# Kernel optimization log

Hardware: AMD Instinct MI355X
Metric: run time of the kernel (lower is better)

## Reference

```python
import jax, jax.numpy as jnp
import numpy as np

PI = 3.14159  # constant used in the torch module
N_QUBITS = 10
N_LAYERS = 4
B = 1024  # number of graphs


def _lin_init(k, fan_in, fan_out):
    k1, k2 = jax.random.split(k)
    s = 1.0 / np.sqrt(fan_in)
    W = jax.random.uniform(k1, (fan_in, fan_out), jnp.float32, -s, s)
    b = jax.random.uniform(k2, (fan_out,), jnp.float32, -s, s)
    return W, b


def setup_inputs():
    key = jax.random.key(0)
    ks = jax.random.split(key, 12)
    N, E, Fin, H, Emb = 32768, 131072, 128, 256, 128
    x = jax.random.normal(ks[0], (N, Fin), jnp.float32)
    edge_index = jax.random.randint(ks[1], (2, E), 0, N)
    batch = jnp.sort(jax.random.randint(ks[2], (N,), 0, B))
    edge_attr = jax.random.uniform(ks[3], (E, 4), dtype=jnp.float32)
    W1, b1 = _lin_init(ks[4], Fin, H)          # GCNConv 1
    W2, b2 = _lin_init(ks[5], H, Emb)          # GCNConv 2
    projW, projb = _lin_init(ks[6], Emb, N_QUBITS)
    vqc_weights = jax.random.uniform(ks[7], (N_LAYERS, N_QUBITS), jnp.float32, 0.0, 2 * np.pi)
    epW, epb = _lin_init(ks[8], 4, N_QUBITS - 1)
    cW1, cb1 = _lin_init(ks[9], Emb + N_QUBITS, 16)
    cW2, cb2 = _lin_init(ks[10], 16, 1)
    return dict(x=x, edge_index=edge_index, batch=batch, edge_attr=edge_attr,
                W1=W1, b1=b1, W2=W2, b2=b2, projW=projW, projb=projb,
                vqc_weights=vqc_weights, epW=epW, epb=epb,
                cW1=cW1, cb1=cb1, cW2=cW2, cb2=cb2)


def _gcn_conv(x, W, b, src, dst, n):
    # GCNConv with self-loops: sym-normalized aggregation of xW
    h = x @ W
    deg = jnp.zeros((n,), x.dtype).at[dst].add(1.0) + 1.0  # +1 self-loop
    dinv = jax.lax.rsqrt(deg)
    coef = (dinv[src] * dinv[dst])[:, None]
    agg = jnp.zeros_like(h).at[dst].add(h[src] * coef)
    return agg + h * (1.0 / deg)[:, None] + b


def _segment_mean(v, seg, n):
    tot = jnp.zeros((n, v.shape[1]), v.dtype).at[seg].add(v)
    cnt = jnp.zeros((n,), v.dtype).at[seg].add(1.0)
    return tot / jnp.clip(cnt, 1.0)[:, None]


def _run_vqc(q_in, weights, ep):
    # Batched real state-vector simulation. All gates (RY, CRY) are real.
    # Wire 0 = most significant bit (pennylane default.qubit convention).
    b = q_in.shape[0]
    dim = 2 ** N_QUBITS
    st = jnp.zeros((b, dim), q_in.dtype).at[:, 0].set(1.0)

    def ry(st, theta, w):
        th = jnp.broadcast_to(theta, (b,)) * 0.5
        c = jnp.cos(th)[:, None, None]
        s = jnp.sin(th)[:, None, None]
        r = st.reshape(b, 2 ** w, 2, -1)
        a0, a1 = r[:, :, 0], r[:, :, 1]
        return jnp.stack([c * a0 - s * a1, s * a0 + c * a1], axis=2).reshape(b, dim)

    def cry(st, theta, w):
        # control w, target w+1 (adjacent wires)
        th = jnp.broadcast_to(theta, (b,)) * 0.5
        c = jnp.cos(th)[:, None, None]
        s = jnp.sin(th)[:, None, None]
        r = st.reshape(b, 2 ** w, 2, 2, -1)
        a0, a1 = r[:, :, 1, 0], r[:, :, 1, 1]
        r = r.at[:, :, 1, 0].set(c * a0 - s * a1).at[:, :, 1, 1].set(s * a0 + c * a1)
        return r.reshape(b, dim)

    for i in range(N_QUBITS):                      # AngleEmbedding (RY)
        st = ry(st, q_in[:, i], i)
    for layer in range(N_LAYERS):
        for i in range(N_QUBITS):
            st = ry(st, weights[layer, i], i)
        for i in range(N_QUBITS - 1):
            st = cry(st, ep[:, i], i)

    probs = st * st
    zs = []
    for i in range(N_QUBITS):
        p = probs.reshape(b, 2 ** i, 2, -1).sum(axis=(1, 3))
        zs.append(p[:, 0] - p[:, 1])               # <PauliZ(i)>
    return jnp.stack(zs, axis=1)                   # [B, n_qubits]


def reference(x, edge_index, batch, edge_attr, W1, b1, W2, b2, projW, projb,
              vqc_weights, epW, epb, cW1, cb1, cW2, cb2):
    N = x.shape[0]
    src, dst = edge_index[0], edge_index[1]
    # GCN encoder: two GCNConv + ReLU, global mean pool (dropout = eval mode)
    h = jax.nn.relu(_gcn_conv(x, W1, b1, src, dst, N))
    h = jax.nn.relu(_gcn_conv(h, W2, b2, src, dst, N))
    emb = _segment_mean(h, batch, B)               # [B, gcn_embed]

    q_in = jnp.tanh(emb @ projW + projb) * PI      # [B, n_qubits]

    # scatter-mean edge pooling per graph, then edge projection
    edge_batch = batch[src]
    pooled_edge = _segment_mean(edge_attr, edge_batch, B)  # [B, 4]
    ep = pooled_edge @ epW + epb                   # [B, n_qubits-1]

    q_out = _run_vqc(q_in, vqc_weights, ep)        # [B, n_qubits]

    combined = jnp.concatenate([emb, q_out], axis=-1)
    hid = jax.nn.relu(combined @ cW1 + cb1)
    return hid @ cW2 + cb2                         # [B, num_tasks]
```

## Files before the change

### kernel.cpp

```cpp
#include <hip/hip_runtime.h>

#define PI_F 3.14159f
#define NQ 10
#define PB 64

__global__ void k_zero(float4* __restrict__ p, int n4) {
  int i = blockIdx.x * blockDim.x + threadIdx.x;
  int stride = gridDim.x * blockDim.x;
  float4 z = {0.f, 0.f, 0.f, 0.f};
  for (; i < n4; i += stride) p[i] = z;
}

__global__ void k_count(const int* __restrict__ dstA, int E, int* __restrict__ cnt) {
  int e = blockIdx.x * blockDim.x + threadIdx.x;
  if (e < E) atomicAdd(&cnt[dstA[e]], 1);
}

__global__ __launch_bounds__(1024) void k_edge_pool(const int* __restrict__ srcA,
                                                    const int* __restrict__ batch,
                                                    const float* __restrict__ eattr, int E,
                                                    float* __restrict__ part) {
  __shared__ float bins[1024 * 5];
  int t = threadIdx.x;
  for (int i = t; i < 5120; i += 1024) bins[i] = 0.f;
  __syncthreads();
  int per = (E + gridDim.x - 1) / gridDim.x;
  int base = blockIdx.x * per;
  int end = min(base + per, E);
  for (int e = base + t; e < end; e += 1024) {
    int s = srcA[e];
    int g = batch[s];
    float4 v = *(const float4*)(eattr + (size_t)e * 4);
    atomicAdd(&bins[g * 5 + 0], v.x);
    atomicAdd(&bins[g * 5 + 1], v.y);
    atomicAdd(&bins[g * 5 + 2], v.z);
    atomicAdd(&bins[g * 5 + 3], v.w);
    atomicAdd(&bins[g * 5 + 4], 1.0f);
  }
  __syncthreads();
  float* dst = part + (size_t)blockIdx.x * 5120;
  for (int i = t; i < 5120; i += 1024) dst[i] = bins[i];
}

__global__ __launch_bounds__(1024) void k_scan1(const int* __restrict__ cnt,
                                                int* __restrict__ incl,
                                                int* __restrict__ bsum) {
  __shared__ int buf[1024];
  int t = threadIdx.x;
  int base = blockIdx.x << 10;
  buf[t] = cnt[base + t];
  __syncthreads();
#pragma unroll
  for (int off = 1; off < 1024; off <<= 1) {
    int x = (t >= off) ? buf[t - off] : 0;
    __syncthreads();
    buf[t] += x;
    __syncthreads();
  }
  incl[base + t] = buf[t];
  if (t == 1023) bsum[blockIdx.x] = buf[t];
}

__global__ void k_node_setup(const int* __restrict__ cnt, const int* __restrict__ incl,
                             const int* __restrict__ bsum, const int* __restrict__ batch,
                             int N, int Bn, int* __restrict__ rowStart,
                             int* __restrict__ pos, float* __restrict__ dinv,
                             float* __restrict__ invdeg, int* __restrict__ starts) {
  int i = blockIdx.x * blockDim.x + threadIdx.x;
  if (i >= N) return;
  int blk = i >> 10;
  int pre = 0;
  for (int j = 0; j < blk; j++) pre += bsum[j];
  int c = cnt[i];
  int inc = incl[i] + pre;
  rowStart[i + 1] = inc;
  pos[i] = inc - c;
  if (i == 0) rowStart[0] = 0;
  float d = (float)c + 1.0f;
  dinv[i] = 1.0f / sqrtf(d);
  invdeg[i] = 1.0f / d;
  int b = batch[i];
  int bp = (i == 0) ? -1 : batch[i - 1];
  for (int g = bp + 1; g <= b; g++) starts[g] = i;
  if (i == N - 1) {
    for (int g = b + 1; g <= Bn; g++) starts[g] = N;
  }
}

__global__ void k_fill(const int* __restrict__ dst, const int* __restrict__ srcA,
                       const float* __restrict__ dinv, int E, int* __restrict__ pos,
                       int* __restrict__ srcSorted, float* __restrict__ dcoef) {
  int e = blockIdx.x * blockDim.x + threadIdx.x;
  if (e >= E) return;
  int s = srcA[e];
  int slot = atomicAdd(&pos[dst[e]], 1);
  srcSorted[slot] = s;
  dcoef[slot] = dinv[s];
}

__global__ __launch_bounds__(256) void k_gemm(const float* __restrict__ A,
                                              const float* __restrict__ B,
                                              float* __restrict__ C,
                                              int M, int K, int N) {
  __shared__ float As[64][36];
  __shared__ float Bs[32][68];
  int t = threadIdx.x;
  int tx = t & 15, ty = t >> 4;
  int row0 = blockIdx.y * 64, col0 = blockIdx.x * 64;
  float acc[4][4] = {};
  for (int k0 = 0; k0 < K; k0 += 32) {
#pragma unroll
    for (int rep = 0; rep < 2; rep++) {
      int slot = t + rep * 256;
      int r = slot >> 3;
      int cg = (slot & 7) << 2;
      float4 v = *(const float4*)(A + (size_t)(row0 + r) * K + (k0 + cg));
      *(float4*)&As[r][cg] = v;
      int r2 = slot >> 4;
      int cg2 = (slot & 15) << 2;
      float4 w = *(const float4*)(B + (size_t)(k0 + r2) * N + (col0 + cg2));
      *(float4*)&Bs[r2][cg2] = w;
    }
    __syncthreads();
#pragma unroll
    for (int kk = 0; kk < 32; kk++) {
      float av[4];
      av[0] = As[ty * 4 + 0][kk];
      av[1] = As[ty * 4 + 1][kk];
      av[2] = As[ty * 4 + 2][kk];
      av[3] = As[ty * 4 + 3][kk];
      float4 b4 = *(const float4*)&Bs[kk][tx << 2];
      float bv[4] = {b4.x, b4.y, b4.z, b4.w};
#pragma unroll
      for (int i = 0; i < 4; i++)
#pragma unroll
        for (int j = 0; j < 4; j++) acc[i][j] = fmaf(av[i], bv[j], acc[i][j]);
    }
    __syncthreads();
  }
#pragma unroll
  for (int i = 0; i < 4; i++) {
    float4 v = {acc[i][0], acc[i][1], acc[i][2], acc[i][3]};
    *(float4*)(C + (size_t)(row0 + ty * 4 + i) * N + (col0 + (tx << 2))) = v;
  }
}

__global__ __launch_bounds__(256) void k_gcn_combine(
    const float* __restrict__ hlin, const int* __restrict__ srcSorted,
    const float* __restrict__ dcoef, const int* __restrict__ rowStart,
    const float* __restrict__ dinv, const float* __restrict__ invdeg,
    const float* __restrict__ bias, float* __restrict__ hout, int N, int C, int shift) {
  int gid = blockIdx.x * blockDim.x + threadIdx.x;
  int n = gid >> shift;
  if (n >= N) return;
  int cq = (gid & ((1 << shift) - 1)) << 2;
  int e0 = rowStart[n], e1 = rowStart[n + 1];
  float di = dinv[n];
  float ax = 0.f, ay = 0.f, az = 0.f, aw = 0.f;
  for (int e = e0; e < e1; e++) {
    int s = srcSorted[e];
    float coef = dcoef[e] * di;
    float4 v = *(const float4*)(hlin + (size_t)s * C + cq);
    ax = fmaf(coef, v.x, ax);
    ay = fmaf(coef, v.y, ay);
    az = fmaf(coef, v.z, az);
    aw = fmaf(coef, v.w, aw);
  }
  float idg = invdeg[n];
  float4 hv = *(const float4*)(hlin + (size_t)n * C + cq);
  float4 bv = *(const float4*)(bias + cq);
  float4 r;
  r.x = fmaxf(fmaf(hv.x, idg, ax) + bv.x, 0.f);
  r.y = fmaxf(fmaf(hv.y, idg, ay) + bv.y, 0.f);
  r.z = fmaxf(fmaf(hv.z, idg, az) + bv.z, 0.f);
  r.w = fmaxf(fmaf(hv.w, idg, aw) + bv.w, 0.f);
  *(float4*)(hout + (size_t)n * C + cq) = r;
}

__global__ __launch_bounds__(256) void k_segmean(const float* __restrict__ h2,
                                                 const int* __restrict__ starts,
                                                 float* __restrict__ emb) {
  __shared__ float tmp[128];
  int g = blockIdx.x;
  int t = threadIdx.x;
  int c = t & 127;
  int half = t >> 7;
  int s0 = starts[g], s1 = starts[g + 1];
  float inv = 1.0f / (float)(s1 - s0 > 0 ? s1 - s0 : 1);
  float sum = 0.f;
  for (int i = s0 + half; i < s1; i += 2) sum += h2[(size_t)i * 128 + c];
  if (half == 0) tmp[c] = sum;
  __syncthreads();
  if (half == 1) emb[(size_t)g * 128 + c] = (tmp[c] + sum) * inv;
}


template <int B>
__device__ __forceinline__ void ry_reg(float* st, float c, float s) {
#pragma unroll
  for (int j = 0; j < 16; j++) {
    if (!(j & (1 << B))) {
      float x0 = st[j], x1 = st[j | (1 << B)];
      st[j] = c * x0 - s * x1;
      st[j | (1 << B)] = fmaf(s, x0, c * x1);
    }
  }
}

template <int LB>
__device__ __forceinline__ void ry_lane(float* st, float c, float s, int lane) {
  bool hi = (lane >> LB) & 1;
#pragma unroll
  for (int j = 0; j < 16; j++) {
    float p = __shfl_xor(st[j], 1 << LB, 64);
    float a = c * st[j] - s * p;
    float b = fmaf(s, p, c * st[j]);
    st[j] = hi ? b : a;
  }
}

template <int LC, int LT>
__device__ __forceinline__ void cry_ll(float* st, float c, float s, int lane) {
  bool ctrl = (lane >> LC) & 1;
  bool hi = (lane >> LT) & 1;
#pragma unroll
  for (int j = 0; j < 16; j++) {
    float p = __shfl_xor(st[j], 1 << LT, 64);
    float a = c * st[j] - s * p;
    float b = fmaf(s, p, c * st[j]);
    float nv = hi ? b : a;
    st[j] = ctrl ? nv : st[j];
  }
}

__device__ __forceinline__ void cry_l0r3(float* st, float c, float s, int lane) {
  bool ctrl = lane & 1;
#pragma unroll
  for (int j = 0; j < 8; j++) {
    float x0 = st[j], x1 = st[j + 8];
    float n0 = c * x0 - s * x1;
    float n1 = fmaf(s, x0, c * x1);
    st[j] = ctrl ? n0 : x0;
    st[j + 8] = ctrl ? n1 : x1;
  }
}

template <int BC, int BT>
__device__ __forceinline__ void cry_rr(float* st, float c, float s) {
#pragma unroll
  for (int j = 0; j < 16; j++) {
    if ((j & (1 << BC)) && !(j & (1 << BT))) {
      float x0 = st[j], x1 = st[j | (1 << BT)];
      st[j] = c * x0 - s * x1;
      st[j | (1 << BT)] = fmaf(s, x0, c * x1);
    }
  }
}

#define RY_LAYER(base)                                    \
  ry_lane<5>(st, csc[(base) + 0], css[(base) + 0], lane); \
  ry_lane<4>(st, csc[(base) + 1], css[(base) + 1], lane); \
  ry_lane<3>(st, csc[(base) + 2], css[(base) + 2], lane); \
  ry_lane<2>(st, csc[(base) + 3], css[(base) + 3], lane); \
  ry_lane<1>(st, csc[(base) + 4], css[(base) + 4], lane); \
  ry_lane<0>(st, csc[(base) + 5], css[(base) + 5], lane); \
  ry_reg<3>(st, csc[(base) + 6], css[(base) + 6]);        \
  ry_reg<2>(st, csc[(base) + 7], css[(base) + 7]);        \
  ry_reg<1>(st, csc[(base) + 8], css[(base) + 8]);        \
  ry_reg<0>(st, csc[(base) + 9], css[(base) + 9]);

#define CRY_LAYER()                            \
  cry_ll<5, 4>(st, csc[50], css[50], lane);    \
  cry_ll<4, 3>(st, csc[51], css[51], lane);    \
  cry_ll<3, 2>(st, csc[52], css[52], lane);    \
  cry_ll<2, 1>(st, csc[53], css[53], lane);    \
  cry_ll<1, 0>(st, csc[54], css[54], lane);    \
  cry_l0r3(st, csc[55], css[55], lane);        \
  cry_rr<3, 2>(st, csc[56], css[56]);          \
  cry_rr<2, 1>(st, csc[57], css[57]);          \
  cry_rr<1, 0>(st, csc[58], css[58]);

__global__ __launch_bounds__(64) void k_vqc_head(
    const float* __restrict__ emb, const float* __restrict__ part,
    const float* __restrict__ projW, const float* __restrict__ projb,
    const float* __restrict__ vqcW, const float* __restrict__ epW,
    const float* __restrict__ epb, const float* __restrict__ cW1,
    const float* __restrict__ cb1, const float* __restrict__ cW2,
    const float* __restrict__ cb2, float* __restrict__ out) {
  int g = blockIdx.x;
  int lane = threadIdx.x;
  __shared__ float semb[128];
  __shared__ float csc[59], css[59];
  __shared__ float pool[5];
  __shared__ float zq[NQ];
  __shared__ float hid[16];

  {
    float2 v = *(const float2*)(emb + (size_t)g * 128 + lane * 2);
    semb[lane * 2] = v.x;
    semb[lane * 2 + 1] = v.y;
  }

  {
    const float* pp = part + (size_t)lane * 5120 + g * 5;
    float p0 = pp[0], p1 = pp[1], p2 = pp[2], p3 = pp[3], p4 = pp[4];
#pragma unroll
    for (int off = 32; off >= 1; off >>= 1) {
      p0 += __shfl_down(p0, off, 64);
      p1 += __shfl_down(p1, off, 64);
      p2 += __shfl_down(p2, off, 64);
      p3 += __shfl_down(p3, off, 64);
      p4 += __shfl_down(p4, off, 64);
    }
    if (lane == 0) {
      pool[0] = p0; pool[1] = p1; pool[2] = p2; pool[3] = p3; pool[4] = p4;
    }
  }
  __syncthreads();

  if (lane < NQ) {
    float sum = projb[lane];
    for (int k = 0; k < 128; k++) sum = fmaf(semb[k], projW[k * NQ + lane], sum);
    float th = tanhf(sum) * PI_F * 0.5f;
    csc[lane] = cosf(th);
    css[lane] = sinf(th);
  } else if (lane < 50) {
    float th = vqcW[lane - NQ] * 0.5f;
    csc[lane] = cosf(th);
    css[lane] = sinf(th);
  } else if (lane < 59) {
    int i = lane - 50;
    float icnt = 1.0f / fmaxf(pool[4], 1.0f);
    float sum = epb[i];
    for (int j = 0; j < 4; j++) sum = fmaf(pool[j] * icnt, epW[j * 9 + i], sum);
    float th = sum * 0.5f;
    csc[lane] = cosf(th);
    css[lane] = sinf(th);
  }
  __syncthreads();

  float st[16];
#pragma unroll
  for (int j = 0; j < 16; j++) st[j] = 0.f;
  if (lane == 0) st[0] = 1.f;

  RY_LAYER(0);
  RY_LAYER(10); CRY_LAYER();
  RY_LAYER(20); CRY_LAYER();
  RY_LAYER(30); CRY_LAYER();
  RY_LAYER(40); CRY_LAYER();

  float p[16];
  float tot = 0.f;
#pragma unroll
  for (int j = 0; j < 16; j++) {
    p[j] = st[j] * st[j];
    tot += p[j];
  }
  float z[NQ];
#pragma unroll
  for (int i = 0; i < 6; i++) {
    int LB = 5 - i;
    z[i] = ((lane >> LB) & 1) ? -tot : tot;
  }
#pragma unroll
  for (int i = 6; i < 10; i++) {
    int B = 9 - i;
    float a = 0.f;
#pragma unroll
    for (int j = 0; j < 16; j++) a += ((j >> B) & 1) ? -p[j] : p[j];
    z[i] = a;
  }
#pragma unroll
  for (int off = 32; off >= 1; off >>= 1)
#pragma unroll
    for (int i = 0; i < 10; i++) z[i] += __shfl_down(z[i], off, 64);
  if (lane == 0) {
#pragma unroll
    for (int i = 0; i < 10; i++) zq[i] = z[i];
  }
  __syncthreads();

  if (lane < 16) {
    float sum = cb1[lane];
    for (int k = 0; k < 128; k++) sum = fmaf(semb[k], cW1[k * 16 + lane], sum);
#pragma unroll
    for (int k = 0; k < 10; k++) sum = fmaf(zq[k], cW1[(128 + k) * 16 + lane], sum);
    hid[lane] = fmaxf(sum, 0.f);
  }
  __syncthreads();
  if (lane == 0) {
    float sum = cb2[0];
#pragma unroll
    for (int j = 0; j < 16; j++) sum = fmaf(hid[j], cW2[j], sum);
    out[g] = sum;
  }
}

extern "C" void kernel_launch(void* const* d_in, const int* in_sizes, int n_in,
                              void* d_out, int out_size, void* d_ws, size_t ws_size,
                              hipStream_t stream) {
  const float* x = (const float*)d_in[0];
  const int* ei = (const int*)d_in[1];
  const int* batch = (const int*)d_in[2];
  const float* eattr = (const float*)d_in[3];
  const float* W1 = (const float*)d_in[4];
  const float* b1 = (const float*)d_in[5];
  const float* W2 = (const float*)d_in[6];
  const float* b2 = (const float*)d_in[7];
  const float* projW = (const float*)d_in[8];
  const float* projb = (const float*)d_in[9];
  const float* vqcW = (const float*)d_in[10];
  const float* epW = (const float*)d_in[11];
  const float* epb = (const float*)d_in[12];
  const float* cW1 = (const float*)d_in[13];
  const float* cb1 = (const float*)d_in[14];
  const float* cW2 = (const float*)d_in[15];
  const float* cb2 = (const float*)d_in[16];
  float* out = (float*)d_out;

  const int N = in_sizes[0] / 128;
  const int E = in_sizes[1] / 2;
  const int Bn = out_size;

  const int* srcA = ei;
  const int* dstA = ei + E;

  char* ws = (char*)d_ws;
  float* bufA = (float*)ws;
  float* bufB = (float*)(ws + ((size_t)32 << 20));
  size_t off = (size_t)64 << 20;
  auto alloc = [&](size_t bytes) {
    size_t o = off;
    off += (bytes + 255) & ~(size_t)255;
    return o;
  };
  int* cnt = (int*)(ws + alloc((size_t)N * 4));
  size_t zeroEnd = off;
  float* part = (float*)(ws + alloc((size_t)PB * 5120 * 4));
  int* rowStart = (int*)(ws + alloc((size_t)(N + 1) * 4));
  int* pos = (int*)(ws + alloc((size_t)N * 4));
  int* srcSorted = (int*)(ws + alloc((size_t)E * 4));
  float* dcoef = (float*)(ws + alloc((size_t)E * 4));
  float* dinv = (float*)(ws + alloc((size_t)N * 4));
  float* invdeg = (float*)(ws + alloc((size_t)N * 4));
  int* starts = (int*)(ws + alloc((size_t)(Bn + 1) * 4));
  int* incl = (int*)(ws + alloc((size_t)N * 4));
  int* bsum = (int*)(ws + alloc(64 * 4));
  float* emb = (float*)(ws + alloc((size_t)Bn * 128 * 4));

  int eblocks = (E + 255) / 256;
  int nblocks = (N + 255) / 256;
  int nb1024 = N >> 10;

  int zero4 = (int)((zeroEnd - ((size_t)64 << 20)) / 16);
  k_zero<<<(zero4 + 255) / 256, 256, 0, stream>>>((float4*)(ws + ((size_t)64 << 20)), zero4);

  k_count<<<eblocks, 256, 0, stream>>>(dstA, E, cnt);
  k_edge_pool<<<PB, 1024, 0, stream>>>(srcA, batch, eattr, E, part);
  k_scan1<<<nb1024, 1024, 0, stream>>>(cnt, incl, bsum);
  k_node_setup<<<nblocks, 256, 0, stream>>>(cnt, incl, bsum, batch, N, Bn, rowStart, pos,
                                            dinv, invdeg, starts);
  k_fill<<<eblocks, 256, 0, stream>>>(dstA, srcA, dinv, E, pos, srcSorted, dcoef);

  {
    dim3 grid(256 / 64, N / 64);
    k_gemm<<<grid, 256, 0, stream>>>(x, W1, bufA, N, 128, 256);
  }
  k_gcn_combine<<<(N * 64) / 256, 256, 0, stream>>>(bufA, srcSorted, dcoef, rowStart,
                                                    dinv, invdeg, b1, bufB, N, 256, 6);
  {
    dim3 grid(128 / 64, N / 64);
    k_gemm<<<grid, 256, 0, stream>>>(bufB, W2, bufA, N, 256, 128);
  }
  k_gcn_combine<<<(N * 32) / 256, 256, 0, stream>>>(bufA, srcSorted, dcoef, rowStart,
                                                    dinv, invdeg, b2, bufB, N, 128, 5);
  k_segmean<<<Bn, 256, 0, stream>>>(bufB, starts, emb);
  k_vqc_head<<<Bn, 64, 0, stream>>>(emb, part, projW, projb, vqcW, epW, epb,
                                    cW1, cb1, cW2, cb2, out);
}
```

Baseline: 202.0 us.

## Split angle computation into wave-parallel kernel and parallelize classifier head

Moves the input projection (128→10 dot products with tanh) and the edge-pool reduction out of the VQC kernel into a new kernel that gives each angle its own wavefront, reducing across lanes with shuffles. The VQC kernel then just loads precomputed cos/sin values. The classifier head is also rewritten so all 64 lanes split the 138-wide dot product and combine with shuffles, replacing the 16-lane serial loop and a block sync. This adds a kernel launch and a small global round trip in exchange for removing serial per-lane loops.

```diff
diff --git a/kernel.cpp b/kernel.cpp
--- a/kernel.cpp
+++ b/kernel.cpp
@@ -194,6 +194,55 @@
   if (half == 1) emb[(size_t)g * 128 + c] = (tmp[c] + sum) * inv;
 }
 
+__global__ __launch_bounds__(256) void k_angles(
+    const float* __restrict__ emb, const float* __restrict__ part,
+    const float* __restrict__ projW, const float* __restrict__ projb,
+    const float* __restrict__ epW, const float* __restrict__ epb, int Bn,
+    float* __restrict__ angc, float* __restrict__ angs) {
+  int wid = (blockIdx.x * blockDim.x + threadIdx.x) >> 6;
+  int lane = threadIdx.x & 63;
+  int g = wid / 11;
+  int a = wid - g * 11;
+  if (g >= Bn) return;
+  if (a < 10) {
+    float2 v = *(const float2*)(emb + (size_t)g * 128 + lane * 2);
+    float s = v.x * projW[(lane * 2) * NQ + a] + v.y * projW[(lane * 2 + 1) * NQ + a];
+#pragma unroll
+    for (int off = 32; off >= 1; off >>= 1) s += __shfl_down(s, off, 64);
+    if (lane == 0) {
+      float th = tanhf(s + projb[a]) * PI_F * 0.5f;
+      angc[g * 19 + a] = cosf(th);
+      angs[g * 19 + a] = sinf(th);
+    }
+  } else {
+    const float* pp = part + (size_t)lane * 5120 + g * 5;
+    float p0 = pp[0], p1 = pp[1], p2 = pp[2], p3 = pp[3], p4 = pp[4];
+#pragma unroll
+    for (int off = 32; off >= 1; off >>= 1) {
+      p0 += __shfl_down(p0, off, 64);
+      p1 += __shfl_down(p1, off, 64);
+      p2 += __shfl_down(p2, off, 64);
+      p3 += __shfl_down(p3, off, 64);
+      p4 += __shfl_down(p4, off, 64);
+    }
+    p0 = __shfl(p0, 0, 64);
+    p1 = __shfl(p1, 0, 64);
+    p2 = __shfl(p2, 0, 64);
+    p3 = __shfl(p3, 0, 64);
+    p4 = __shfl(p4, 0, 64);
+    if (lane < 9) {
+      float icnt = 1.0f / fmaxf(p4, 1.0f);
+      float sum = epb[lane];
+      sum = fmaf(p0 * icnt, epW[0 * 9 + lane], sum);
+      sum = fmaf(p1 * icnt, epW[1 * 9 + lane], sum);
+      sum = fmaf(p2 * icnt, epW[2 * 9 + lane], sum);
+      sum = fmaf(p3 * icnt, epW[3 * 9 + lane], sum);
+      float th = sum * 0.5f;
+      angc[g * 19 + 10 + lane] = cosf(th);
+      angs[g * 19 + 10 + lane] = sinf(th);
+    }
+  }
+}
 
 template <int B>
 __device__ __forceinline__ void ry_reg(float* st, float c, float s) {
@@ -281,61 +330,32 @@
   cry_rr<1, 0>(st, csc[58], css[58]);
 
 __global__ __launch_bounds__(64) void k_vqc_head(
-    const float* __restrict__ emb, const float* __restrict__ part,
-    const float* __restrict__ projW, const float* __restrict__ projb,
-    const float* __restrict__ vqcW, const float* __restrict__ epW,
-    const float* __restrict__ epb, const float* __restrict__ cW1,
-    const float* __restrict__ cb1, const float* __restrict__ cW2,
-    const float* __restrict__ cb2, float* __restrict__ out) {
+    const float* __restrict__ emb, const float* __restrict__ angc,
+    const float* __restrict__ angs, const float* __restrict__ vqcW,
+    const float* __restrict__ cW1, const float* __restrict__ cb1,
+    const float* __restrict__ cW2, const float* __restrict__ cb2,
+    float* __restrict__ out) {
   int g = blockIdx.x;
   int lane = threadIdx.x;
   __shared__ float semb[128];
   __shared__ float csc[59], css[59];
-  __shared__ float pool[5];
   __shared__ float zq[NQ];
-  __shared__ float hid[16];
 
   {
     float2 v = *(const float2*)(emb + (size_t)g * 128 + lane * 2);
     semb[lane * 2] = v.x;
     semb[lane * 2 + 1] = v.y;
   }
-
-  {
-    const float* pp = part + (size_t)lane * 5120 + g * 5;
-    float p0 = pp[0], p1 = pp[1], p2 = pp[2], p3 = pp[3], p4 = pp[4];
-#pragma unroll
-    for (int off = 32; off >= 1; off >>= 1) {
-      p0 += __shfl_down(p0, off, 64);
-      p1 += __shfl_down(p1, off, 64);
-      p2 += __shfl_down(p2, off, 64);
-      p3 += __shfl_down(p3, off, 64);
-      p4 += __shfl_down(p4, off, 64);
-    }
-    if (lane == 0) {
-      pool[0] = p0; pool[1] = p1; pool[2] = p2; pool[3] = p3; pool[4] = p4;
-    }
-  }
-  __syncthreads();
-
   if (lane < NQ) {
-    float sum = projb[lane];
-    for (int k = 0; k < 128; k++) sum = fmaf(semb[k], projW[k * NQ + lane], sum);
-    float th = tanhf(sum) * PI_F * 0.5f;
-    csc[lane] = cosf(th);
-    css[lane] = sinf(th);
+    csc[lane] = angc[g * 19 + lane];
+    css[lane] = angs[g * 19 + lane];
   } else if (lane < 50) {
     float th = vqcW[lane - NQ] * 0.5f;
     csc[lane] = cosf(th);
     css[lane] = sinf(th);
   } else if (lane < 59) {
-    int i = lane - 50;
-    float icnt = 1.0f / fmaxf(pool[4], 1.0f);
-    float sum = epb[i];
-    for (int j = 0; j < 4; j++) sum = fmaf(pool[j] * icnt, epW[j * 9 + i], sum);
-    float th = sum * 0.5f;
-    csc[lane] = cosf(th);
-    css[lane] = sinf(th);
+    csc[lane] = angc[g * 19 + 10 + (lane - 50)];
+    css[lane] = angs[g * 19 + 10 + (lane - 50)];
   }
   __syncthreads();
 
@@ -381,20 +401,26 @@
   }
   __syncthreads();
 
-  if (lane < 16) {
-    float sum = cb1[lane];
-    for (int k = 0; k < 128; k++) sum = fmaf(semb[k], cW1[k * 16 + lane], sum);
-#pragma unroll
-    for (int k = 0; k < 10; k++) sum = fmaf(zq[k], cW1[(128 + k) * 16 + lane], sum);
-    hid[lane] = fmaxf(sum, 0.f);
-  }
-  __syncthreads();
-  if (lane == 0) {
-    float sum = cb2[0];
-#pragma unroll
-    for (int j = 0; j < 16; j++) sum = fmaf(hid[j], cW2[j], sum);
-    out[g] = sum;
-  }
+  int o = lane & 15, cch = lane >> 4;
+  float sum = 0.f;
+#pragma unroll
+  for (int t = 0; t < 32; t++) {
+    int k = cch * 32 + t;
+    sum = fmaf(semb[k], cW1[k * 16 + o], sum);
+  }
+  if (cch == 3) {
+#pragma unroll
+    for (int k = 0; k < 10; k++) sum = fmaf(zq[k], cW1[(128 + k) * 16 + o], sum);
+  }
+  sum += __shfl_down(sum, 32, 64);
+  sum += __shfl_down(sum, 16, 64);
+  float hv = fmaxf(sum + cb1[o], 0.f);
+  float ov = (lane < 16) ? hv * cW2[lane] : 0.f;
+  ov += __shfl_down(ov, 8, 64);
+  ov += __shfl_down(ov, 4, 64);
+  ov += __shfl_down(ov, 2, 64);
+  ov += __shfl_down(ov, 1, 64);
+  if (lane == 0) out[g] = ov + cb2[0];
 }
 
 extern "C" void kernel_launch(void* const* d_in, const int* in_sizes, int n_in,
@@ -448,6 +474,8 @@
   int* incl = (int*)(ws + alloc((size_t)N * 4));
   int* bsum = (int*)(ws + alloc(64 * 4));
   float* emb = (float*)(ws + alloc((size_t)Bn * 128 * 4));
+  float* angc = (float*)(ws + alloc((size_t)Bn * 19 * 4));
+  float* angs = (float*)(ws + alloc((size_t)Bn * 19 * 4));
 
   int eblocks = (E + 255) / 256;
   int nblocks = (N + 255) / 256;
@@ -476,6 +504,10 @@
   k_gcn_combine<<<(N * 32) / 256, 256, 0, stream>>>(bufA, srcSorted, dcoef, rowStart,
                                                     dinv, invdeg, b2, bufB, N, 128, 5);
   k_segmean<<<Bn, 256, 0, stream>>>(bufB, starts, emb);
-  k_vqc_head<<<Bn, 64, 0, stream>>>(emb, part, projW, projb, vqcW, epW, epb,
-                                    cW1, cb1, cW2, cb2, out);
-}
+  {
+    int waves = Bn * 11;
+    k_angles<<<(waves + 3) / 4, 256, 0, stream>>>(emb, part, projW, projb, epW, epb, Bn,
+                                                  angc, angs);
+  }
+  k_vqc_head<<<Bn, 64, 0, stream>>>(emb, angc, angs, vqcW, cW1, cb1, cW2, cb2, out);
+}
```

New measurement: 199.7 us. No clear change (-1.2%).
